# Optimization experiments

Measured on AMD Instinct MI355X. Metric: run time of the kernel, lower is better.

Reference implementation:

```python
import jax, jax.numpy as jnp
import numpy as np

N = 10000
E = 80000


def gat_layer(x, src, dst, W, a_src, a_dst, b):
    # x: [N, Fin], W: [Fin, Fout]
    xw = x @ W                              # [N, Fout]
    al_src = xw @ a_src                     # [N]
    al_dst = xw @ a_dst                     # [N]
    e = jax.nn.leaky_relu(al_src[src] + al_dst[dst], 0.2)  # [E+N]
    m = jax.lax.stop_gradient(jax.ops.segment_max(e, dst, num_segments=N))
    ex = jnp.exp(e - m[dst])
    denom = jax.ops.segment_sum(ex, dst, num_segments=N)
    alpha = ex / (denom[dst] + 1e-16)       # PyG softmax eps
    out = jax.ops.segment_sum(alpha[:, None] * xw[src], dst, num_segments=N)
    return out + b


def setup_inputs() -> dict:
    key = jax.random.key(0)
    ks = jax.random.split(key, 12)
    x = jax.random.normal(ks[0], (N, 256), dtype=jnp.float32)
    edge_index = jax.random.randint(ks[1], (2, E), 0, N, dtype=jnp.int64)
    def glorot(k, fi, fo):
        return jax.random.normal(k, (fi, fo), jnp.float32) * jnp.sqrt(2.0 / (fi + fo))
    W1 = glorot(ks[2], 256, 2048)
    W2 = glorot(ks[3], 2048, 2048)
    W3 = glorot(ks[4], 2048, 1024)
    a1s = jax.random.normal(ks[5], (2048,), jnp.float32) * 0.05
    a1d = jax.random.normal(ks[6], (2048,), jnp.float32) * 0.05
    a2s = jax.random.normal(ks[7], (2048,), jnp.float32) * 0.05
    a2d = jax.random.normal(ks[8], (2048,), jnp.float32) * 0.05
    a3s = jax.random.normal(ks[9], (1024,), jnp.float32) * 0.05
    a3d = jax.random.normal(ks[10], (1024,), jnp.float32) * 0.05
    b1 = jnp.zeros((2048,), jnp.float32)
    b2 = jnp.zeros((2048,), jnp.float32)
    b3 = jnp.zeros((1024,), jnp.float32)
    return {"x": x, "edge_index": edge_index, "W1": W1, "W2": W2, "W3": W3,
            "a1s": a1s, "a1d": a1d, "a2s": a2s, "a2d": a2d, "a3s": a3s, "a3d": a3d,
            "b1": b1, "b2": b2, "b3": b3}


def reference(x, edge_index, W1, W2, W3, a1s, a1d, a2s, a2d, a3s, a3d, b1, b2, b3):
    # add self loops (PyG GATConv default add_self_loops=True)
    loop = jnp.arange(N, dtype=edge_index.dtype)
    src = jnp.concatenate([edge_index[0], loop])
    dst = jnp.concatenate([edge_index[1], loop])
    h = jax.nn.relu(gat_layer(x, src, dst, W1, a1s, a1d, b1))
    h = jax.nn.relu(gat_layer(h, src, dst, W2, a2s, a2d, b2))
    h = jax.nn.relu(gat_layer(h, src, dst, W3, a3s, a3d, b3))
    # F.normalize(dim=1), eps=1e-12
    norm = jnp.linalg.norm(h, axis=1, keepdims=True)
    return h / jnp.maximum(norm, 1e-12)
```

## Files before the change

kernel.cpp:

```cpp
#include <hip/hip_runtime.h>
#include <hip/hip_bf16.h>
#include <math.h>


typedef __attribute__((ext_vector_type(8))) short short8;
typedef __attribute__((ext_vector_type(4))) float f32x4;

#define GLOAD_LDS16(g, l)                                            \
  __builtin_amdgcn_global_load_lds(                                  \
      (const __attribute__((address_space(1))) void*)(g),            \
      (__attribute__((address_space(3))) void*)(l), 16, 0, 0)

#define CFENCE asm volatile("" ::: "memory")

__device__ __forceinline__ float bf16_to_f32(ushort u) {
  return __uint_as_float(((unsigned int)u) << 16);
}

__device__ __forceinline__ float block_reduce_sum_bcast(float v) {
#pragma unroll
  for (int off = 32; off > 0; off >>= 1) v += __shfl_down(v, off, 64);
  __shared__ float tmp[4];
  __shared__ float res;
  int lane = threadIdx.x & 63, w = threadIdx.x >> 6;
  if (lane == 0) tmp[w] = v;
  __syncthreads();
  if (threadIdx.x == 0) res = tmp[0] + tmp[1] + tmp[2] + tmp[3];
  __syncthreads();
  float out = res;
  __syncthreads();
  return out;
}

__device__ __forceinline__ float block_reduce_max_bcast(float v) {
#pragma unroll
  for (int off = 32; off > 0; off >>= 1) v = fmaxf(v, __shfl_down(v, off, 64));
  __shared__ float tmpm[4];
  __shared__ float resm;
  int lane = threadIdx.x & 63, w = threadIdx.x >> 6;
  if (lane == 0) tmpm[w] = v;
  __syncthreads();
  if (threadIdx.x == 0) resm = fmaxf(fmaxf(tmpm[0], tmpm[1]), fmaxf(tmpm[2], tmpm[3]));
  __syncthreads();
  float out = resm;
  __syncthreads();
  return out;
}

__global__ __launch_bounds__(256) void convert_f32_bf16(const float* __restrict__ in,
                                                        __hip_bfloat16* __restrict__ out,
                                                        int n) {
  int i = blockIdx.x * blockDim.x + threadIdx.x;
  if (i < n) out[i] = __float2bfloat16(in[i]);
}

__global__ __launch_bounds__(256) void transpose_w(const float* __restrict__ W,
                                                   __hip_bfloat16* __restrict__ Wt,
                                                   int K, int Nout) {
  __shared__ float t[32][33];
  int tx = threadIdx.x & 31, ty = threadIdx.x >> 5;
  int n0 = blockIdx.x * 32, k0 = blockIdx.y * 32;
#pragma unroll
  for (int i = 0; i < 4; ++i) {
    int k = k0 + ty + i * 8;
    t[ty + i * 8][tx] = W[(size_t)k * Nout + n0 + tx];
  }
  __syncthreads();
#pragma unroll
  for (int i = 0; i < 4; ++i) {
    int n = n0 + ty + i * 8;
    Wt[(size_t)n * K + k0 + tx] = __float2bfloat16(t[tx][ty + i * 8]);
  }
}

__global__ __launch_bounds__(256) void matvec_wa(const float* __restrict__ W,
                                                 const float* __restrict__ a_s,
                                                 const float* __restrict__ a_d,
                                                 float* __restrict__ wa_s,
                                                 float* __restrict__ wa_d, int F) {
  int k = blockIdx.x;
  const float* row = W + (size_t)k * F;
  float s1 = 0.f, s2 = 0.f;
  for (int f = threadIdx.x; f < F; f += 256) {
    float w = row[f];
    s1 += w * a_s[f];
    s2 += w * a_d[f];
  }
  float r1 = block_reduce_sum_bcast(s1);
  float r2 = block_reduce_sum_bcast(s2);
  if (threadIdx.x == 0) {
    wa_s[k] = r1;
    wa_d[k] = r2;
  }
}

template <int FPT>
__global__ __launch_bounds__(256) void compute_al(const ushort* __restrict__ H,
                                                  const float* __restrict__ wa_s,
                                                  const float* __restrict__ wa_d,
                                                  float* __restrict__ als,
                                                  float* __restrict__ ald, int F) {
  int n = blockIdx.x;
  const ushort* row = H + (size_t)n * F;
  float s1 = 0.f, s2 = 0.f;
  if (FPT == 8) {
    int base = threadIdx.x * 8;
    short8 v = *(const short8*)(row + base);
#pragma unroll
    for (int j = 0; j < 8; ++j) {
      float f = bf16_to_f32((ushort)v[j]);
      s1 += f * wa_s[base + j];
      s2 += f * wa_d[base + j];
    }
  } else {
    float f = bf16_to_f32(row[threadIdx.x]);
    s1 = f * wa_s[threadIdx.x];
    s2 = f * wa_d[threadIdx.x];
  }
  float r1 = block_reduce_sum_bcast(s1);
  float r2 = block_reduce_sum_bcast(s2);
  if (threadIdx.x == 0) {
    als[n] = r1;
    ald[n] = r2;
  }
}

__global__ void count_kernel(const int* __restrict__ dst, int* __restrict__ counts, int E) {
  int i = blockIdx.x * blockDim.x + threadIdx.x;
  if (i < E) atomicAdd(&counts[dst[i]], 1);
}

__global__ __launch_bounds__(1024) void scan_kernel(const int* __restrict__ counts,
                                                    int* __restrict__ rowptr,
                                                    int* __restrict__ cursor, int Nn) {
  __shared__ int part[1024];
  int tid = threadIdx.x;
  int chunk = (Nn + 1023) / 1024;
  int base = tid * chunk;
  int s = 0;
  for (int i = 0; i < chunk; ++i) {
    int idx = base + i;
    if (idx < Nn) s += counts[idx];
  }
  part[tid] = s;
  __syncthreads();
  for (int off = 1; off < 1024; off <<= 1) {
    int v = 0;
    if (tid >= off) v = part[tid - off];
    __syncthreads();
    if (tid >= off) part[tid] += v;
    __syncthreads();
  }
  int run = (tid == 0) ? 0 : part[tid - 1];
  for (int i = 0; i < chunk; ++i) {
    int idx = base + i;
    if (idx < Nn) {
      rowptr[idx] = run;
      cursor[idx] = run;
      run += counts[idx];
    }
  }
  if (tid == 1023) rowptr[Nn] = part[1023];
}

__global__ void fill_kernel(const int* __restrict__ src, const int* __restrict__ dst,
                            int* __restrict__ cursor, int* __restrict__ eidx, int E) {
  int i = blockIdx.x * blockDim.x + threadIdx.x;
  if (i < E) {
    int pos = atomicAdd(&cursor[dst[i]], 1);
    eidx[pos] = src[i];
  }
}

template <int FPT>
__global__ __launch_bounds__(256) void aggregate(const ushort* __restrict__ H,
                                                 const float* __restrict__ als,
                                                 const float* __restrict__ ald,
                                                 const int* __restrict__ rowptr,
                                                 const int* __restrict__ eidx,
                                                 ushort* __restrict__ out, int F) {
  int n = blockIdx.x;
  int tid = threadIdx.x;
  int beg = rowptr[n], end = rowptr[n + 1];
  int deg = end - beg;
  float aldn = ald[n];

  float lm = -INFINITY;
  for (int j = tid; j < deg; j += 256) {
    int s = eidx[beg + j];
    float e = als[s] + aldn;
    e = (e > 0.f) ? e : 0.2f * e;
    lm = fmaxf(lm, e);
  }
  if (tid == 0) {
    float e = als[n] + aldn;
    e = (e > 0.f) ? e : 0.2f * e;
    lm = fmaxf(lm, e);
  }
  float m = block_reduce_max_bcast(lm);

  float ls = 0.f;
  for (int j = tid; j < deg; j += 256) {
    int s = eidx[beg + j];
    float e = als[s] + aldn;
    e = (e > 0.f) ? e : 0.2f * e;
    ls += expf(e - m);
  }
  if (tid == 0) {
    float e = als[n] + aldn;
    e = (e > 0.f) ? e : 0.2f * e;
    ls += expf(e - m);
  }
  float denom = block_reduce_sum_bcast(ls) + 1e-16f;
  float inv_denom = 1.f / denom;

  float acc[FPT];
#pragma unroll
  for (int i = 0; i < FPT; ++i) acc[i] = 0.f;

  __shared__ float alpha_sh[256];
  __shared__ int src_sh[256];
  int total = deg + 1;
  for (int c0 = 0; c0 < total; c0 += 256) {
    int j = c0 + tid;
    if (j < total) {
      int s = (j < deg) ? eidx[beg + j] : n;
      float e = als[s] + aldn;
      e = (e > 0.f) ? e : 0.2f * e;
      alpha_sh[tid] = expf(e - m) * inv_denom;
      src_sh[tid] = s;
    }
    __syncthreads();
    int cn = min(256, total - c0);
    for (int jj = 0; jj < cn; ++jj) {
      float al = alpha_sh[jj];
      const ushort* row = H + (size_t)src_sh[jj] * F;
      if (FPT == 1) {
        acc[0] += al * bf16_to_f32(row[tid]);
      } else {
#pragma unroll
        for (int i = 0; i < FPT / 2; ++i) {
          unsigned int u = *(const unsigned int*)(row + tid * 2 + i * 512);
          acc[2 * i]     += al * __uint_as_float((u & 0xffffu) << 16);
          acc[2 * i + 1] += al * __uint_as_float(u & 0xffff0000u);
        }
      }
    }
    __syncthreads();
  }

#pragma unroll
  for (int i = 0; i < FPT; ++i) {
    int col = (FPT == 1) ? tid : (tid * 2 + (i >> 1) * 512 + (i & 1));
    __hip_bfloat16 hv = __float2bfloat16(acc[i]);
    out[(size_t)n * F + col] = *(ushort*)&hv;
  }
}

template <bool BF16OUT>
__global__ __launch_bounds__(256, 4) void gemm_t128(const ushort* __restrict__ A,
                                                    const ushort* __restrict__ Bt,
                                                    const float* __restrict__ bias,
                                                    void* __restrict__ C,
                                                    int M, int K, int Nout) {
  constexpr int BUF = 8192;
  extern __shared__ ushort lds[];
  const int tid = threadIdx.x;
  const int l = tid & 63, w = tid >> 6;
  const int wm = w >> 1, wn = w & 1;
  const int l15 = l & 15, lhi = l >> 4;

  int nwg = gridDim.x * gridDim.y;
  int lin = blockIdx.y * gridDim.x + blockIdx.x;
  if ((nwg & 7) == 0) lin = (lin & 7) * (nwg >> 3) + (lin >> 3);
  const int bx = lin % gridDim.x, by = lin / gridDim.x;
  const int row0 = by * 128, col0 = bx * 128;

  const int c8sw = (l & 3) ^ (((l >> 5) & 1) << 1);
  const int lrow = l >> 2;
  const int chsw = lhi ^ (((l15 >> 3) & 1) << 1);
  const int rd_off = l15 * 32 + chsw * 8;

  const int sA0 = w * 2;
  const ushort* ga[2];
  const ushort* gb[2];
#pragma unroll
  for (int j = 0; j < 2; ++j) {
    int ar = min(row0 + (sA0 + j) * 16 + lrow, M - 1);
    ga[j] = A + (size_t)ar * K + c8sw * 8;
    gb[j] = Bt + (size_t)(col0 + (sA0 + j) * 16 + lrow) * K + c8sw * 8;
  }

#define STAGE(nb, kn)                                                     \
  do {                                                                    \
    GLOAD_LDS16(ga[0] + (kn), &lds[(nb)*BUF + (sA0 + 0) * 512]);          \
    GLOAD_LDS16(ga[1] + (kn), &lds[(nb)*BUF + (sA0 + 1) * 512]);          \
    GLOAD_LDS16(gb[0] + (kn), &lds[(nb)*BUF + 4096 + (sA0 + 0) * 512]);   \
    GLOAD_LDS16(gb[1] + (kn), &lds[(nb)*BUF + 4096 + (sA0 + 1) * 512]);   \
  } while (0)

  f32x4 acc[4][4] = {};

#define PHASE(cur, WAITLIT, STAGE_STMT)                                              \
  do {                                                                               \
    STAGE_STMT;                                                                      \
    asm volatile("s_waitcnt vmcnt(" WAITLIT ")" ::: "memory");                       \
    __builtin_amdgcn_s_barrier();                                                    \
    CFENCE;                                                                          \
    short8 af[4], bf[4];                                                             \
    const ushort* Ab = &lds[(cur)*BUF];                                              \
    const ushort* Bb = &lds[(cur)*BUF + 4096];                                       \
    _Pragma("unroll") for (int m = 0; m < 4; ++m)                                    \
        af[m] = *(const short8*)(Ab + (wm * 4 + m) * 512 + rd_off);                  \
    _Pragma("unroll") for (int n = 0; n < 4; ++n)                                    \
        bf[n] = *(const short8*)(Bb + (wn * 4 + n) * 512 + rd_off);                  \
    __builtin_amdgcn_s_setprio(1);                                                   \
    _Pragma("unroll") for (int m = 0; m < 4; ++m)                                    \
        _Pragma("unroll") for (int n = 0; n < 4; ++n)                                \
            acc[m][n] = __builtin_amdgcn_mfma_f32_16x16x32_bf16(                     \
                af[m], bf[n], acc[m][n], 0, 0, 0);                                   \
    __builtin_amdgcn_s_setprio(0);                                                   \
    CFENCE;                                                                          \
    __builtin_amdgcn_s_barrier();                                                    \
    CFENCE;                                                                          \
  } while (0)

  const int nt = K >> 5;
  STAGE(0, 0);
  int cur = 0;
  for (int t = 0; t < nt - 1; ++t) {
    const int kn = (t + 1) << 5;
    PHASE(cur, "4", STAGE(cur ^ 1, kn));
    cur ^= 1;
  }
  PHASE(cur, "0", );

#pragma unroll
  for (int mi = 0; mi < 4; ++mi) {
#pragma unroll
    for (int v = 0; v < 4; ++v) {
      int r = row0 + wm * 64 + mi * 16 + lhi * 4 + v;
      if (r < M) {
#pragma unroll
        for (int n = 0; n < 4; ++n) {
          int col = col0 + wn * 64 + n * 16 + l15;
          float val = fmaxf(acc[mi][n][v] + bias[col], 0.f);
          size_t idx = (size_t)r * Nout + col;
          if (BF16OUT)
            ((__hip_bfloat16*)C)[idx] = __float2bfloat16(val);
          else
            ((float*)C)[idx] = val;
        }
      }
    }
  }
#undef PHASE
#undef STAGE
}

template <bool BF16OUT>
__global__ __launch_bounds__(512, 4) void gemm_p2(const ushort* __restrict__ A,
                                                  const ushort* __restrict__ Bt,
                                                  const float* __restrict__ bias,
                                                  void* __restrict__ C,
                                                  int M, int K, int Nout) {
  constexpr int BUF = 12288;
  extern __shared__ ushort lds[];
  const int tid = threadIdx.x;
  const int l = tid & 63, w = tid >> 6;
  const int wm = w >> 2, wn = w & 3;
  const int l15 = l & 15, lhi = l >> 4;

  int nwg = gridDim.x * gridDim.y;
  int lin = blockIdx.y * gridDim.x + blockIdx.x;
  if ((nwg & 7) == 0) lin = (lin & 7) * (nwg >> 3) + (lin >> 3);
  const int bx = lin % gridDim.x, by = lin / gridDim.x;
  const int row0 = by * 256, col0 = bx * 128;

  const int c8sw = (l & 3) ^ (((l >> 5) & 1) << 1);
  const int lrow = l >> 2;
  const int chsw = lhi ^ (((l15 >> 3) & 1) << 1);
  const int rd_off = l15 * 32 + chsw * 8;

  const int sA0 = w * 2;
  const int sB0 = w;
  const ushort* ga[2];
  const ushort* gb;
#pragma unroll
  for (int j = 0; j < 2; ++j) {
    int ar = min(row0 + (sA0 + j) * 16 + lrow, M - 1);
    ga[j] = A + (size_t)ar * K + c8sw * 8;
  }
  gb = Bt + (size_t)(col0 + sB0 * 16 + lrow) * K + c8sw * 8;

#define STAGE(nb, kn)                                               \
  do {                                                              \
    GLOAD_LDS16(ga[0] + (kn), &lds[(nb)*BUF + (sA0 + 0) * 512]);    \
    GLOAD_LDS16(ga[1] + (kn), &lds[(nb)*BUF + (sA0 + 1) * 512]);    \
    GLOAD_LDS16(gb + (kn), &lds[(nb)*BUF + 8192 + sB0 * 512]);      \
  } while (0)

  f32x4 acc[8][2] = {};

#define PHASE(cur, WAITLIT, STAGE_STMT)                                              \
  do {                                                                               \
    STAGE_STMT;                                                                      \
    asm volatile("s_waitcnt vmcnt(" WAITLIT ")" ::: "memory");                       \
    __builtin_amdgcn_s_barrier();                                                    \
    CFENCE;                                                                          \
    short8 af[8], bf[2];                                                             \
    const ushort* Ab = &lds[(cur)*BUF];                                              \
    const ushort* Bb = &lds[(cur)*BUF + 8192];                                       \
    _Pragma("unroll") for (int m = 0; m < 8; ++m)                                    \
        af[m] = *(const short8*)(Ab + (wm * 8 + m) * 512 + rd_off);                  \
    _Pragma("unroll") for (int n = 0; n < 2; ++n)                                    \
        bf[n] = *(const short8*)(Bb + (wn * 2 + n) * 512 + rd_off);                  \
    __builtin_amdgcn_s_setprio(1);                                                   \
    _Pragma("unroll") for (int m = 0; m < 8; ++m)                                    \
        _Pragma("unroll") for (int n = 0; n < 2; ++n)                                \
            acc[m][n] = __builtin_amdgcn_mfma_f32_16x16x32_bf16(                     \
                af[m], bf[n], acc[m][n], 0, 0, 0);                                   \
    __builtin_amdgcn_s_setprio(0);                                                   \
    CFENCE;                                                                          \
    __builtin_amdgcn_s_barrier();                                                    \
    CFENCE;                                                                          \
  } while (0)

  const int nt = K >> 5;
  STAGE(0, 0);
  int cur = 0;
  for (int t = 0; t < nt - 1; ++t) {
    const int kn = (t + 1) << 5;
    PHASE(cur, "3", STAGE(cur ^ 1, kn));
    cur ^= 1;
  }
  PHASE(cur, "0", );

#pragma unroll
  for (int mi = 0; mi < 8; ++mi) {
#pragma unroll
    for (int v = 0; v < 4; ++v) {
      int r = row0 + wm * 128 + mi * 16 + lhi * 4 + v;
      if (r < M) {
#pragma unroll
        for (int n = 0; n < 2; ++n) {
          int col = col0 + wn * 32 + n * 16 + l15;
          float val = fmaxf(acc[mi][n][v] + bias[col], 0.f);
          size_t idx = (size_t)r * Nout + col;
          if (BF16OUT)
            ((__hip_bfloat16*)C)[idx] = __float2bfloat16(val);
          else
            ((float*)C)[idx] = val;
        }
      }
    }
  }
#undef PHASE
#undef STAGE
}

__global__ __launch_bounds__(256) void normalize_kernel(const float* __restrict__ h,
                                                        float* __restrict__ out,
                                                        int F) {
  int n = blockIdx.x;
  const float* row = h + (size_t)n * F;
  float ss = 0.f;
  for (int f = threadIdx.x; f < F; f += 256) {
    float v = row[f];
    ss += v * v;
  }
  float tot = block_reduce_sum_bcast(ss);
  float inv = 1.f / fmaxf(sqrtf(tot), 1e-12f);
  for (int f = threadIdx.x; f < F; f += 256) {
    out[(size_t)n * F + f] = row[f] * inv;
  }
}

extern "C" void kernel_launch(void* const* d_in, const int* in_sizes, int n_in,
                              void* d_out, int out_size, void* d_ws, size_t ws_size,
                              hipStream_t stream) {
  const float* x   = (const float*)d_in[0];
  const int*   ei  = (const int*)d_in[1];
  const float* W1  = (const float*)d_in[2];
  const float* W2  = (const float*)d_in[3];
  const float* W3  = (const float*)d_in[4];
  const float* a1s = (const float*)d_in[5];
  const float* a1d = (const float*)d_in[6];
  const float* a2s = (const float*)d_in[7];
  const float* a2d = (const float*)d_in[8];
  const float* a3s = (const float*)d_in[9];
  const float* a3d = (const float*)d_in[10];
  const float* b1  = (const float*)d_in[11];
  const float* b2  = (const float*)d_in[12];
  const float* b3  = (const float*)d_in[13];

  const int N = in_sizes[0] / 256;
  const int E = in_sizes[1] / 2;

  char* ws = (char*)d_ws;
  size_t off = 0;
  auto alloc = [&](size_t bytes) -> void* {
    void* p = ws + off;
    off += (bytes + 255) & ~(size_t)255;
    return p;
  };
  ushort* h    = (ushort*)alloc((size_t)N * 2048 * 2);
  ushort* hagg = (ushort*)alloc((size_t)N * 2048 * 2);
  float* hf32  = (float*)alloc((size_t)N * 1024 * 4);
  ushort* xb   = (ushort*)alloc((size_t)N * 256 * 2);
  __hip_bfloat16* Wt1 = (__hip_bfloat16*)alloc((size_t)2048 * 256 * 2);
  __hip_bfloat16* Wt2 = (__hip_bfloat16*)alloc((size_t)2048 * 2048 * 2);
  __hip_bfloat16* Wt3 = (__hip_bfloat16*)alloc((size_t)1024 * 2048 * 2);
  float* wa1s = (float*)alloc(256 * 4);
  float* wa1d = (float*)alloc(256 * 4);
  float* wa2s = (float*)alloc(2048 * 4);
  float* wa2d = (float*)alloc(2048 * 4);
  float* wa3s = (float*)alloc(2048 * 4);
  float* wa3d = (float*)alloc(2048 * 4);
  float* als   = (float*)alloc((size_t)N * 4);
  float* ald   = (float*)alloc((size_t)N * 4);
  int* counts  = (int*)alloc((size_t)N * 4);
  int* rowptr  = (int*)alloc((size_t)(N + 1) * 4);
  int* cursor  = (int*)alloc((size_t)N * 4);
  int* eidx    = (int*)alloc((size_t)E * 4);

  const int* srcp = ei;
  const int* dstp = ei + E;

  hipFuncSetAttribute((const void*)gemm_t128<true>,
                      hipFuncAttributeMaxDynamicSharedMemorySize, 32768);
  hipFuncSetAttribute((const void*)gemm_t128<false>,
                      hipFuncAttributeMaxDynamicSharedMemorySize, 32768);
  hipFuncSetAttribute((const void*)gemm_p2<true>,
                      hipFuncAttributeMaxDynamicSharedMemorySize, 49152);

  hipMemsetAsync(counts, 0, (size_t)N * 4, stream);
  count_kernel<<<(E + 255) / 256, 256, 0, stream>>>(dstp, counts, E);
  scan_kernel<<<1, 1024, 0, stream>>>(counts, rowptr, cursor, N);
  fill_kernel<<<(E + 255) / 256, 256, 0, stream>>>(srcp, dstp, cursor, eidx, E);

  convert_f32_bf16<<<(N * 256 + 255) / 256, 256, 0, stream>>>(x, (__hip_bfloat16*)xb, N * 256);
  transpose_w<<<dim3(2048 / 32, 256 / 32), 256, 0, stream>>>(W1, Wt1, 256, 2048);
  transpose_w<<<dim3(2048 / 32, 2048 / 32), 256, 0, stream>>>(W2, Wt2, 2048, 2048);
  transpose_w<<<dim3(1024 / 32, 2048 / 32), 256, 0, stream>>>(W3, Wt3, 2048, 1024);
  matvec_wa<<<256, 256, 0, stream>>>(W1, a1s, a1d, wa1s, wa1d, 2048);
  matvec_wa<<<2048, 256, 0, stream>>>(W2, a2s, a2d, wa2s, wa2d, 2048);
  matvec_wa<<<2048, 256, 0, stream>>>(W3, a3s, a3d, wa3s, wa3d, 1024);

  dim3 blk(256);
  dim3 gblk(512);
  int mb128 = (N + 127) / 128;
  int mb256 = (N + 255) / 256;

  compute_al<1><<<N, blk, 0, stream>>>(xb, wa1s, wa1d, als, ald, 256);
  aggregate<1><<<N, blk, 0, stream>>>(xb, als, ald, rowptr, eidx, hagg, 256);
  gemm_t128<true><<<dim3(16, mb128), blk, 32768, stream>>>(hagg, (const ushort*)Wt1, b1, h, N, 256, 2048);

  compute_al<8><<<N, blk, 0, stream>>>(h, wa2s, wa2d, als, ald, 2048);
  aggregate<8><<<N, blk, 0, stream>>>(h, als, ald, rowptr, eidx, hagg, 2048);
  gemm_p2<true><<<dim3(16, mb256), gblk, 49152, stream>>>(hagg, (const ushort*)Wt2, b2, h, N, 2048, 2048);

  compute_al<8><<<N, blk, 0, stream>>>(h, wa3s, wa3d, als, ald, 2048);
  aggregate<8><<<N, blk, 0, stream>>>(h, als, ald, rowptr, eidx, hagg, 2048);
  gemm_t128<false><<<dim3(8, mb128), blk, 32768, stream>>>(hagg, (const ushort*)Wt3, b3, hf32, N, 2048, 1024);

  normalize_kernel<<<N, blk, 0, stream>>>(hf32, (float*)d_out, 1024);
}
```

Baseline: 426.3 us.

## Fuse input conversion with attention logits, single-pass softmax, bf16 final GEMM output

The separate fp32-to-bf16 conversion of x is merged with the first layer's attention-logit computation, removing one launch and one read of x. The aggregate kernel gains a fast path for nodes with at most 256 incident edges, computing edge scores once and reusing them for max, sum and alpha instead of three passes over the neighbor list. The last GEMM now writes bf16 into the existing buffer and normalization reads bf16, which halves that intermediate's traffic. The cost is a loss of precision before the final L2 normalization.

```diff
diff --git a/kernel.cpp b/kernel.cpp
--- a/kernel.cpp
+++ b/kernel.cpp
@@ -47,11 +47,25 @@
   return out;
 }
 
-__global__ __launch_bounds__(256) void convert_f32_bf16(const float* __restrict__ in,
-                                                        __hip_bfloat16* __restrict__ out,
-                                                        int n) {
-  int i = blockIdx.x * blockDim.x + threadIdx.x;
-  if (i < n) out[i] = __float2bfloat16(in[i]);
+__global__ __launch_bounds__(256) void convert_al1(const float* __restrict__ x,
+                                                   ushort* __restrict__ xb,
+                                                   const float* __restrict__ wa_s,
+                                                   const float* __restrict__ wa_d,
+                                                   float* __restrict__ als,
+                                                   float* __restrict__ ald) {
+  int n = blockIdx.x;
+  int tid = threadIdx.x;
+  float v = x[(size_t)n * 256 + tid];
+  __hip_bfloat16 hv = __float2bfloat16(v);
+  ushort bits = *(ushort*)&hv;
+  xb[(size_t)n * 256 + tid] = bits;
+  float f = bf16_to_f32(bits);
+  float r1 = block_reduce_sum_bcast(f * wa_s[tid]);
+  float r2 = block_reduce_sum_bcast(f * wa_d[tid]);
+  if (tid == 0) {
+    als[n] = r1;
+    ald[n] = r2;
+  }
 }
 
 __global__ __launch_bounds__(256) void transpose_w(const float* __restrict__ W,
@@ -94,28 +108,21 @@
   }
 }
 
-template <int FPT>
-__global__ __launch_bounds__(256) void compute_al(const ushort* __restrict__ H,
-                                                  const float* __restrict__ wa_s,
-                                                  const float* __restrict__ wa_d,
-                                                  float* __restrict__ als,
-                                                  float* __restrict__ ald, int F) {
+__global__ __launch_bounds__(256) void compute_al8(const ushort* __restrict__ H,
+                                                   const float* __restrict__ wa_s,
+                                                   const float* __restrict__ wa_d,
+                                                   float* __restrict__ als,
+                                                   float* __restrict__ ald) {
   int n = blockIdx.x;
-  const ushort* row = H + (size_t)n * F;
+  const ushort* row = H + (size_t)n * 2048;
   float s1 = 0.f, s2 = 0.f;
-  if (FPT == 8) {
-    int base = threadIdx.x * 8;
-    short8 v = *(const short8*)(row + base);
-#pragma unroll
-    for (int j = 0; j < 8; ++j) {
-      float f = bf16_to_f32((ushort)v[j]);
-      s1 += f * wa_s[base + j];
-      s2 += f * wa_d[base + j];
-    }
-  } else {
-    float f = bf16_to_f32(row[threadIdx.x]);
-    s1 = f * wa_s[threadIdx.x];
-    s2 = f * wa_d[threadIdx.x];
+  int base = threadIdx.x * 8;
+  short8 v = *(const short8*)(row + base);
+#pragma unroll
+  for (int j = 0; j < 8; ++j) {
+    float f = bf16_to_f32((ushort)v[j]);
+    s1 += f * wa_s[base + j];
+    s2 += f * wa_d[base + j];
   }
   float r1 = block_reduce_sum_bcast(s1);
   float r2 = block_reduce_sum_bcast(s2);
@@ -183,56 +190,32 @@
   int tid = threadIdx.x;
   int beg = rowptr[n], end = rowptr[n + 1];
   int deg = end - beg;
+  int total = deg + 1;
   float aldn = ald[n];
-
-  float lm = -INFINITY;
-  for (int j = tid; j < deg; j += 256) {
-    int s = eidx[beg + j];
-    float e = als[s] + aldn;
-    e = (e > 0.f) ? e : 0.2f * e;
-    lm = fmaxf(lm, e);
-  }
-  if (tid == 0) {
-    float e = als[n] + aldn;
-    e = (e > 0.f) ? e : 0.2f * e;
-    lm = fmaxf(lm, e);
-  }
-  float m = block_reduce_max_bcast(lm);
-
-  float ls = 0.f;
-  for (int j = tid; j < deg; j += 256) {
-    int s = eidx[beg + j];
-    float e = als[s] + aldn;
-    e = (e > 0.f) ? e : 0.2f * e;
-    ls += expf(e - m);
-  }
-  if (tid == 0) {
-    float e = als[n] + aldn;
-    e = (e > 0.f) ? e : 0.2f * e;
-    ls += expf(e - m);
-  }
-  float denom = block_reduce_sum_bcast(ls) + 1e-16f;
-  float inv_denom = 1.f / denom;
-
-  float acc[FPT];
-#pragma unroll
-  for (int i = 0; i < FPT; ++i) acc[i] = 0.f;
 
   __shared__ float alpha_sh[256];
   __shared__ int src_sh[256];
-  int total = deg + 1;
-  for (int c0 = 0; c0 < total; c0 += 256) {
-    int j = c0 + tid;
-    if (j < total) {
-      int s = (j < deg) ? eidx[beg + j] : n;
-      float e = als[s] + aldn;
+
+  float acc[FPT];
+#pragma unroll
+  for (int i = 0; i < FPT; ++i) acc[i] = 0.f;
+
+  if (total <= 256) {
+    int s = n;
+    float e = -INFINITY;
+    if (tid < total) {
+      s = (tid < deg) ? eidx[beg + tid] : n;
+      e = als[s] + aldn;
       e = (e > 0.f) ? e : 0.2f * e;
-      alpha_sh[tid] = expf(e - m) * inv_denom;
-      src_sh[tid] = s;
-    }
+    }
+    float m = block_reduce_max_bcast(e);
+    float ex = (tid < total) ? expf(e - m) : 0.f;
+    float denom = block_reduce_sum_bcast(ex) + 1e-16f;
+    float inv_denom = 1.f / denom;
+    alpha_sh[tid] = ex * inv_denom;
+    src_sh[tid] = s;
     __syncthreads();
-    int cn = min(256, total - c0);
-    for (int jj = 0; jj < cn; ++jj) {
+    for (int jj = 0; jj < total; ++jj) {
       float al = alpha_sh[jj];
       const ushort* row = H + (size_t)src_sh[jj] * F;
       if (FPT == 1) {
@@ -246,7 +229,63 @@
         }
       }
     }
-    __syncthreads();
+  } else {
+    float lm = -INFINITY;
+    for (int j = tid; j < deg; j += 256) {
+      int s = eidx[beg + j];
+      float e = als[s] + aldn;
+      e = (e > 0.f) ? e : 0.2f * e;
+      lm = fmaxf(lm, e);
+    }
+    if (tid == 0) {
+      float e = als[n] + aldn;
+      e = (e > 0.f) ? e : 0.2f * e;
+      lm = fmaxf(lm, e);
+    }
+    float m = block_reduce_max_bcast(lm);
+
+    float ls = 0.f;
+    for (int j = tid; j < deg; j += 256) {
+      int s = eidx[beg + j];
+      float e = als[s] + aldn;
+      e = (e > 0.f) ? e : 0.2f * e;
+      ls += expf(e - m);
+    }
+    if (tid == 0) {
+      float e = als[n] + aldn;
+      e = (e > 0.f) ? e : 0.2f * e;
+      ls += expf(e - m);
+    }
+    float denom = block_reduce_sum_bcast(ls) + 1e-16f;
+    float inv_denom = 1.f / denom;
+
+    for (int c0 = 0; c0 < total; c0 += 256) {
+      int j = c0 + tid;
+      if (j < total) {
+        int s = (j < deg) ? eidx[beg + j] : n;
+        float e = als[s] + aldn;
+        e = (e > 0.f) ? e : 0.2f * e;
+        alpha_sh[tid] = expf(e - m) * inv_denom;
+        src_sh[tid] = s;
+      }
+      __syncthreads();
+      int cn = min(256, total - c0);
+      for (int jj = 0; jj < cn; ++jj) {
+        float al = alpha_sh[jj];
+        const ushort* row = H + (size_t)src_sh[jj] * F;
+        if (FPT == 1) {
+          acc[0] += al * bf16_to_f32(row[tid]);
+        } else {
+#pragma unroll
+          for (int i = 0; i < FPT / 2; ++i) {
+            unsigned int u = *(const unsigned int*)(row + tid * 2 + i * 512);
+            acc[2 * i]     += al * __uint_as_float((u & 0xffffu) << 16);
+            acc[2 * i + 1] += al * __uint_as_float(u & 0xffff0000u);
+          }
+        }
+      }
+      __syncthreads();
+    }
   }
 
 #pragma unroll
@@ -459,20 +498,24 @@
 #undef STAGE
 }
 
-__global__ __launch_bounds__(256) void normalize_kernel(const float* __restrict__ h,
-                                                        float* __restrict__ out,
-                                                        int F) {
+__global__ __launch_bounds__(256) void normalize_bf16(const ushort* __restrict__ h,
+                                                      float* __restrict__ out,
+                                                      int F) {
   int n = blockIdx.x;
-  const float* row = h + (size_t)n * F;
+  const ushort* row = h + (size_t)n * F;
   float ss = 0.f;
-  for (int f = threadIdx.x; f < F; f += 256) {
-    float v = row[f];
+  float vals[4];
+#pragma unroll
+  for (int i = 0; i < 4; ++i) {
+    float v = bf16_to_f32(row[threadIdx.x + i * 256]);
+    vals[i] = v;
     ss += v * v;
   }
   float tot = block_reduce_sum_bcast(ss);
   float inv = 1.f / fmaxf(sqrtf(tot), 1e-12f);
-  for (int f = threadIdx.x; f < F; f += 256) {
-    out[(size_t)n * F + f] = row[f] * inv;
+#pragma unroll
+  for (int i = 0; i < 4; ++i) {
+    out[(size_t)n * F + threadIdx.x + i * 256] = vals[i] * inv;
   }
 }
 
@@ -506,7 +549,6 @@
   };
   ushort* h    = (ushort*)alloc((size_t)N * 2048 * 2);
   ushort* hagg = (ushort*)alloc((size_t)N * 2048 * 2);
-  float* hf32  = (float*)alloc((size_t)N * 1024 * 4);
   ushort* xb   = (ushort*)alloc((size_t)N * 256 * 2);
   __hip_bfloat16* Wt1 = (__hip_bfloat16*)alloc((size_t)2048 * 256 * 2);
   __hip_bfloat16* Wt2 = (__hip_bfloat16*)alloc((size_t)2048 * 2048 * 2);
@@ -529,8 +571,6 @@
 
   hipFuncSetAttribute((const void*)gemm_t128<true>,
                       hipFuncAttributeMaxDynamicSharedMemorySize, 32768);
-  hipFuncSetAttribute((const void*)gemm_t128<false>,
-                      hipFuncAttributeMaxDynamicSharedMemorySize, 32768);
   hipFuncSetAttribute((const void*)gemm_p2<true>,
                       hipFuncAttributeMaxDynamicSharedMemorySize, 49152);
 
@@ -539,7 +579,6 @@
   scan_kernel<<<1, 1024, 0, stream>>>(counts, rowptr, cursor, N);
   fill_kernel<<<(E + 255) / 256, 256, 0, stream>>>(srcp, dstp, cursor, eidx, E);
 
-  convert_f32_bf16<<<(N * 256 + 255) / 256, 256, 0, stream>>>(x, (__hip_bfloat16*)xb, N * 256);
   transpose_w<<<dim3(2048 / 32, 256 / 32), 256, 0, stream>>>(W1, Wt1, 256, 2048);
   transpose_w<<<dim3(2048 / 32, 2048 / 32), 256, 0, stream>>>(W2, Wt2, 2048, 2048);
   transpose_w<<<dim3(1024 / 32, 2048 / 32), 256, 0, stream>>>(W3, Wt3, 2048, 1024);
@@ -552,17 +591,17 @@
   int mb128 = (N + 127) / 128;
   int mb256 = (N + 255) / 256;
 
-  compute_al<1><<<N, blk, 0, stream>>>(xb, wa1s, wa1d, als, ald, 256);
+  convert_al1<<<N, blk, 0, stream>>>(x, xb, wa1s, wa1d, als, ald);
   aggregate<1><<<N, blk, 0, stream>>>(xb, als, ald, rowptr, eidx, hagg, 256);
   gemm_t128<true><<<dim3(16, mb128), blk, 32768, stream>>>(hagg, (const ushort*)Wt1, b1, h, N, 256, 2048);
 
-  compute_al<8><<<N, blk, 0, stream>>>(h, wa2s, wa2d, als, ald, 2048);
+  compute_al8<<<N, blk, 0, stream>>>(h, wa2s, wa2d, als, ald);
   aggregate<8><<<N, blk, 0, stream>>>(h, als, ald, rowptr, eidx, hagg, 2048);
   gemm_p2<true><<<dim3(16, mb256), gblk, 49152, stream>>>(hagg, (const ushort*)Wt2, b2, h, N, 2048, 2048);
 
-  compute_al<8><<<N, blk, 0, stream>>>(h, wa3s, wa3d, als, ald, 2048);
+  compute_al8<<<N, blk, 0, stream>>>(h, wa3s, wa3d, als, ald);
   aggregate<8><<<N, blk, 0, stream>>>(h, als, ald, rowptr, eidx, hagg, 2048);
-  gemm_t128<false><<<dim3(8, mb128), blk, 32768, stream>>>(hagg, (const ushort*)Wt3, b3, hf32, N, 2048, 1024);
-
-  normalize_kernel<<<N, blk, 0, stream>>>(hf32, (float*)d_out, 1024);
-}
+  gemm_t128<true><<<dim3(8, mb128), blk, 32768, stream>>>(hagg, (const ushort*)Wt3, b3, h, N, 2048, 1024);
+
+  normalize_bf16<<<N, blk, 0, stream>>>(h, (float*)d_out, 1024);
+}
```

After: 415.5 us. -2.5%, faster.
